# Optimization experiments

Measured on AMD Instinct MI355X. Metric: run time of the kernel, lower is better.

The kernel has to match this reference:

```python
import jax, jax.numpy as jnp
import numpy as np

N_NODES = 50000

def sage_conv(x, src, dst, W_l, b_l, W_r):
    # mean-aggregate neighbor features x[src] at dst, then lin_l(agg)+lin_r(x)
    msgs = x[src]                                       # [E, d]
    agg = jax.ops.segment_sum(msgs, dst, num_segments=N_NODES)
    cnt = jax.ops.segment_sum(jnp.ones((src.shape[0],), x.dtype), dst, num_segments=N_NODES)
    agg = agg / jnp.maximum(cnt, 1.0)[:, None]          # [N, d]
    return agg @ W_l.T + b_l + x @ W_r.T


def setup_inputs() -> dict:
    key = jax.random.key(0)
    ks = jax.random.split(key, 10)
    in_c, hid, out_c = 128, 128, 64
    x = jax.random.normal(ks[0], (N_NODES, in_c), dtype=jnp.float32)
    edge_index = jax.random.randint(ks[1], (2, 800000), 0, N_NODES, dtype=jnp.int64)
    s = 1.0 / np.sqrt(in_c)
    W1_l = jax.random.uniform(ks[2], (hid, in_c), minval=-s, maxval=s)
    b1 = jax.random.uniform(ks[3], (hid,), minval=-s, maxval=s)
    W1_r = jax.random.uniform(ks[4], (hid, in_c), minval=-s, maxval=s)
    s = 1.0 / np.sqrt(hid)
    W2_l = jax.random.uniform(ks[5], (hid, hid), minval=-s, maxval=s)
    b2 = jax.random.uniform(ks[6], (hid,), minval=-s, maxval=s)
    W2_r = jax.random.uniform(ks[7], (hid, hid), minval=-s, maxval=s)
    W3 = jax.random.uniform(ks[8], (out_c, hid), minval=-s, maxval=s)
    b3 = jax.random.uniform(ks[9], (out_c,), minval=-s, maxval=s)
    return {"x": x, "edge_index": edge_index, "W1_l": W1_l, "b1": b1, "W1_r": W1_r,
            "W2_l": W2_l, "b2": b2, "W2_r": W2_r, "W3": W3, "b3": b3}


def reference(x, edge_index, W1_l, b1, W1_r, W2_l, b2, W2_r, W3, b3):
    src, dst = edge_index[0], edge_index[1]
    h = jax.nn.relu(sage_conv(x, src, dst, W1_l, b1, W1_r))
    h = jax.nn.relu(sage_conv(h, src, dst, W2_l, b2, W2_r))
    return h @ W3.T + b3
```

## Files before the change

### kernel.cpp

```cpp
#include <hip/hip_runtime.h>

#define FDIM 128

typedef __attribute__((ext_vector_type(8))) short bf16x8;
typedef __attribute__((ext_vector_type(4))) float f32x4;

static __device__ __forceinline__ ushort f2bf(float f) {
    uint u = __float_as_uint(f);
    uint r = (u + 0x7FFF + ((u >> 16) & 1)) >> 16;
    return (ushort)r;
}
static __device__ __forceinline__ uint packbf(float lo, float hi) {
    return (uint)f2bf(lo) | ((uint)f2bf(hi) << 16);
}
static __device__ __forceinline__ float bflo(uint v) { return __uint_as_float(v << 16); }
static __device__ __forceinline__ float bfhi(uint v) { return __uint_as_float(v & 0xFFFF0000u); }

#define ACC8(A, V) do { \
    A[0] += bflo((V).x); A[1] += bfhi((V).x); \
    A[2] += bflo((V).y); A[3] += bfhi((V).y); \
    A[4] += bflo((V).z); A[5] += bfhi((V).z); \
    A[6] += bflo((V).w); A[7] += bfhi((V).w); } while (0)


__global__ void prep_kernel(const float* __restrict__ x, ushort* __restrict__ xb, int nx8,
                            const float* __restrict__ W1l, const float* __restrict__ W1r,
                            const float* __restrict__ W2l, const float* __restrict__ W2r,
                            const float* __restrict__ W3, ushort* __restrict__ wbuf,
                            const int* __restrict__ dst, int E, int* __restrict__ bcnt,
                            int* __restrict__ hdone, int* __restrict__ bbase,
                            int* __restrict__ bcur, int nb, int nconv, int nhist) {
    const int b = blockIdx.x;
    const int tid = threadIdx.x;
    if (b < nconv) {
        int i = b * 256 + tid;
        if (i < nx8) {
            const float* s = x + (size_t)i * 8;
            float4 a = *(const float4*)(s);
            float4 c = *(const float4*)(s + 4);
            uint4 o;
            o.x = packbf(a.x, a.y); o.y = packbf(a.z, a.w);
            o.z = packbf(c.x, c.y); o.w = packbf(c.z, c.w);
            *(uint4*)(xb + (size_t)i * 8) = o;
        }
    } else if (b < nconv + 36) {
        int c = (b - nconv) * 256 + tid;
        const float* s; ushort* d;
        if (c < 2048)      { s = W1l + (size_t)c * 8;          d = wbuf + (size_t)c * 8; }
        else if (c < 4096) { s = W1r + (size_t)(c - 2048) * 8; d = wbuf + 16384 + (size_t)(c - 2048) * 8; }
        else if (c < 6144) { s = W2l + (size_t)(c - 4096) * 8; d = wbuf + 32768 + (size_t)(c - 4096) * 8; }
        else if (c < 8192) { s = W2r + (size_t)(c - 6144) * 8; d = wbuf + 49152 + (size_t)(c - 6144) * 8; }
        else               { s = W3  + (size_t)(c - 8192) * 8; d = wbuf + 65536 + (size_t)(c - 8192) * 8; }
        float4 a = *(const float4*)(s);
        float4 cc = *(const float4*)(s + 4);
        uint4 o;
        o.x = packbf(a.x, a.y); o.y = packbf(a.z, a.w);
        o.z = packbf(cc.x, cc.y); o.w = packbf(cc.z, cc.w);
        *(uint4*)d = o;
    } else {
        __shared__ int lh[256];
        __shared__ int isLast;
        int hb = b - nconv - 36;
        lh[tid] = 0;
        __syncthreads();
        #pragma unroll
        for (int k = 0; k < 8; ++k) {
            int e = hb * 2048 + k * 256 + tid;
            if (e < E) atomicAdd(&lh[dst[e] >> 8], 1);
        }
        __syncthreads();
        if (lh[tid]) atomicAdd(&bcnt[tid], lh[tid]);
        __syncthreads();
        if (tid == 0) {
            __threadfence();
            isLast = (atomicAdd(hdone, 1) == nhist - 1);
        }
        __syncthreads();
        if (isLast && tid < 64) {
            __threadfence();
            volatile int* vb = bcnt;
            const int i0 = tid * 4;
            int v0 = (i0 + 0 < nb) ? vb[i0 + 0] : 0;
            int v1 = (i0 + 1 < nb) ? vb[i0 + 1] : 0;
            int v2 = (i0 + 2 < nb) ? vb[i0 + 2] : 0;
            int v3 = (i0 + 3 < nb) ? vb[i0 + 3] : 0;
            int s = v0 + v1 + v2 + v3;
            int incl = s;
            #pragma unroll
            for (int d = 1; d < 64; d <<= 1) {
                int t = __shfl_up(incl, d);
                if (tid >= d) incl += t;
            }
            int excl = incl - s;
            int e0 = excl, e1 = excl + v0, e2 = e1 + v1, e3 = e2 + v2;
            if (i0 + 0 < nb) { bbase[i0 + 0] = e0; bcur[i0 + 0] = e0; }
            if (i0 + 1 < nb) { bbase[i0 + 1] = e1; bcur[i0 + 1] = e1; }
            if (i0 + 2 < nb) { bbase[i0 + 2] = e2; bcur[i0 + 2] = e2; }
            if (i0 + 3 < nb) { bbase[i0 + 3] = e3; bcur[i0 + 3] = e3; }
            int total = __shfl(incl, 63);
            if (tid == 0) bbase[nb] = total;
        }
    }
}


__global__ void pair_scatter(const int* __restrict__ src, const int* __restrict__ dst,
                             int* __restrict__ bcur, uint* __restrict__ pairs, int E) {
    __shared__ int lh[256];
    __shared__ int gb[256];
    const int tid = threadIdx.x;
    lh[tid] = 0;
    __syncthreads();
    int ss[8], dd[8], sl[8];
    #pragma unroll
    for (int k = 0; k < 8; ++k) {
        int e = blockIdx.x * 2048 + k * 256 + tid;
        if (e < E) {
            ss[k] = src[e];
            dd[k] = dst[e];
            sl[k] = atomicAdd(&lh[dd[k] >> 8], 1);
        } else dd[k] = -1;
    }
    __syncthreads();
    if (lh[tid]) gb[tid] = atomicAdd(&bcur[tid], lh[tid]);
    __syncthreads();
    #pragma unroll
    for (int k = 0; k < 8; ++k) {
        if (dd[k] >= 0)
            pairs[gb[dd[k] >> 8] + sl[k]] = (uint)ss[k] | ((uint)(dd[k] & 255) << 24);
    }
}


__global__ void bucket_csr(const uint* __restrict__ pairs, const int* __restrict__ bbase,
                           int* __restrict__ off, int* __restrict__ csr, int N) {
    __shared__ int cnt[256];
    __shared__ int base[256];
    __shared__ int cur[256];
    const int b = blockIdx.x;
    const int tid = threadIdx.x;
    const int p0 = bbase[b], p1 = bbase[b + 1];
    cnt[tid] = 0;
    __syncthreads();
    for (int p = p0 + tid; p < p1; p += 256) atomicAdd(&cnt[pairs[p] >> 24], 1);
    __syncthreads();
    if (tid < 64) {
        int i0 = tid * 4;
        int v0 = cnt[i0], v1 = cnt[i0 + 1], v2 = cnt[i0 + 2], v3 = cnt[i0 + 3];
        int s = v0 + v1 + v2 + v3;
        int incl = s;
        #pragma unroll
        for (int d = 1; d < 64; d <<= 1) {
            int t = __shfl_up(incl, d);
            if (tid >= d) incl += t;
        }
        int excl = incl - s;
        base[i0] = excl; base[i0 + 1] = excl + v0;
        base[i0 + 2] = excl + v0 + v1; base[i0 + 3] = excl + v0 + v1 + v2;
        cur[i0] = base[i0]; cur[i0 + 1] = base[i0 + 1];
        cur[i0 + 2] = base[i0 + 2]; cur[i0 + 3] = base[i0 + 3];
    }
    __syncthreads();
    int node = (b << 8) + tid;
    if (node <= N) off[node] = p0 + base[tid];
    for (int p = p0 + tid; p < p1; p += 256) {
        uint e = pairs[p];
        int slot = atomicAdd(&cur[e >> 24], 1);
        csr[p0 + slot] = (int)(e & 0xFFFFFF);
    }
}


template<int HEAD>
__global__ void fused_sage(const ushort* __restrict__ feat, const int* __restrict__ off,
                           const int* __restrict__ csr,
                           const ushort* __restrict__ Wl, const ushort* __restrict__ Wr,
                           const float* __restrict__ bias,
                           const ushort* __restrict__ W3, const float* __restrict__ b3,
                           ushort* __restrict__ hout, float* __restrict__ fout, int n) {
    __shared__ __align__(16) ushort As[32 * FDIM];
    __shared__ __align__(16) ushort Xs[32 * FDIM];
    const int row0 = blockIdx.x * 32;
    const int lane = threadIdx.x & 63;
    const int wid  = threadIdx.x >> 6;

    const int offv = off[min(row0 + wid * 8 + min(lane, 8), n)];

    const float4 z4 = make_float4(0.f, 0.f, 0.f, 0.f);
    #pragma unroll
    for (int i = 0; i < 2; ++i) {
        int s = threadIdx.x + i * 256;
        int r = s >> 4, cch = s & 15;
        int row = row0 + r;
        float4 vx = (row < n) ? *(const float4*)(feat + (size_t)row * FDIM + cch * 8) : z4;
        *(float4*)(Xs + (r * 16 + (cch ^ (r & 7))) * 8) = vx;
    }

    const int g = lane >> 4;
    const int c = lane & 15;
    #define LDROW(s) (*(const uint4*)(feat + (size_t)(s) * FDIM + c * 8))

    #pragma unroll
    for (int i = 0; i < 4; ++i) {
        const int rA = wid * 8 + 2 * i;
        const int nodeA = row0 + rA, nodeB = nodeA + 1;
        const int j0A = __shfl(offv, 2 * i), j1A = __shfl(offv, 2 * i + 1);
        const int j1B = __shfl(offv, 2 * i + 2);
        float a[8] = {0.f, 0.f, 0.f, 0.f, 0.f, 0.f, 0.f, 0.f};
        float bacc[8] = {0.f, 0.f, 0.f, 0.f, 0.f, 0.f, 0.f, 0.f};
        int jA = j0A + g, jB = j1A + g;
        for (; jA + 12 < j1A && jB + 12 < j1B; jA += 16, jB += 16) {
            int sA0 = csr[jA], sA1 = csr[jA + 4], sA2 = csr[jA + 8], sA3 = csr[jA + 12];
            int sB0 = csr[jB], sB1 = csr[jB + 4], sB2 = csr[jB + 8], sB3 = csr[jB + 12];
            uint4 vA0 = LDROW(sA0), vA1 = LDROW(sA1), vA2 = LDROW(sA2), vA3 = LDROW(sA3);
            uint4 vB0 = LDROW(sB0), vB1 = LDROW(sB1), vB2 = LDROW(sB2), vB3 = LDROW(sB3);
            ACC8(a, vA0); ACC8(a, vA1); ACC8(a, vA2); ACC8(a, vA3);
            ACC8(bacc, vB0); ACC8(bacc, vB1); ACC8(bacc, vB2); ACC8(bacc, vB3);
        }
        for (; jA + 12 < j1A; jA += 16) {
            int s0 = csr[jA], s1 = csr[jA + 4], s2 = csr[jA + 8], s3 = csr[jA + 12];
            uint4 v0 = LDROW(s0), v1 = LDROW(s1), v2 = LDROW(s2), v3 = LDROW(s3);
            ACC8(a, v0); ACC8(a, v1); ACC8(a, v2); ACC8(a, v3);
        }
        for (; jA + 4 < j1A; jA += 8) {
            int s0 = csr[jA], s1 = csr[jA + 4];
            uint4 v0 = LDROW(s0), v1 = LDROW(s1);
            ACC8(a, v0); ACC8(a, v1);
        }
        for (; jA < j1A; jA += 4) {
            int s0 = csr[jA];
            uint4 v0 = LDROW(s0);
            ACC8(a, v0);
        }
        for (; jB + 12 < j1B; jB += 16) {
            int s0 = csr[jB], s1 = csr[jB + 4], s2 = csr[jB + 8], s3 = csr[jB + 12];
            uint4 v0 = LDROW(s0), v1 = LDROW(s1), v2 = LDROW(s2), v3 = LDROW(s3);
            ACC8(bacc, v0); ACC8(bacc, v1); ACC8(bacc, v2); ACC8(bacc, v3);
        }
        for (; jB + 4 < j1B; jB += 8) {
            int s0 = csr[jB], s1 = csr[jB + 4];
            uint4 v0 = LDROW(s0), v1 = LDROW(s1);
            ACC8(bacc, v0); ACC8(bacc, v1);
        }
        for (; jB < j1B; jB += 4) {
            int s0 = csr[jB];
            uint4 v0 = LDROW(s0);
            ACC8(bacc, v0);
        }
        #pragma unroll
        for (int k = 0; k < 8; ++k) {
            a[k] += __shfl_xor(a[k], 16);
            bacc[k] += __shfl_xor(bacc[k], 16);
            a[k] += __shfl_xor(a[k], 32);
            bacc[k] += __shfl_xor(bacc[k], 32);
        }
        if (g == 0) {
            float invA = (nodeA < n) ? 1.0f / fmaxf((float)(j1A - j0A), 1.0f) : 0.f;
            float invB = (nodeB < n) ? 1.0f / fmaxf((float)(j1B - j1A), 1.0f) : 0.f;
            uint4 oA, oB;
            oA.x = packbf(a[0] * invA, a[1] * invA);
            oA.y = packbf(a[2] * invA, a[3] * invA);
            oA.z = packbf(a[4] * invA, a[5] * invA);
            oA.w = packbf(a[6] * invA, a[7] * invA);
            oB.x = packbf(bacc[0] * invB, bacc[1] * invB);
            oB.y = packbf(bacc[2] * invB, bacc[3] * invB);
            oB.z = packbf(bacc[4] * invB, bacc[5] * invB);
            oB.w = packbf(bacc[6] * invB, bacc[7] * invB);
            *(uint4*)(As + (rA * 16 + (c ^ (rA & 7))) * 8) = oA;
            *(uint4*)(As + ((rA + 1) * 16 + (c ^ ((rA + 1) & 7))) * 8) = oB;
        }
    }
    #undef LDROW
    __syncthreads();

    const int wrow = wid & 1;
    const int wcol = wid >> 1;
    const int lr = lane & 15;
    const int lk = lane >> 4;

    f32x4 acc[4];
    #pragma unroll
    for (int t = 0; t < 4; ++t) acc[t] = (f32x4){0.f, 0.f, 0.f, 0.f};

    const int arow = wrow * 16 + lr;
    #pragma unroll
    for (int ks = 0; ks < 4; ++ks) {
        bf16x8 a = *(const bf16x8*)(As + (arow * 16 + ((ks * 4 + lk) ^ (arow & 7))) * 8);
        #pragma unroll
        for (int t = 0; t < 4; ++t) {
            int wr = wcol * 64 + t * 16 + lr;
            bf16x8 bb = *(const bf16x8*)(Wl + (size_t)wr * FDIM + ks * 32 + lk * 8);
            acc[t] = __builtin_amdgcn_mfma_f32_16x16x32_bf16(a, bb, acc[t], 0, 0, 0);
        }
    }
    #pragma unroll
    for (int ks = 0; ks < 4; ++ks) {
        bf16x8 a = *(const bf16x8*)(Xs + (arow * 16 + ((ks * 4 + lk) ^ (arow & 7))) * 8);
        #pragma unroll
        for (int t = 0; t < 4; ++t) {
            int wr = wcol * 64 + t * 16 + lr;
            bf16x8 bb = *(const bf16x8*)(Wr + (size_t)wr * FDIM + ks * 32 + lk * 8);
            acc[t] = __builtin_amdgcn_mfma_f32_16x16x32_bf16(a, bb, acc[t], 0, 0, 0);
        }
    }

    if (HEAD == 0) {
        #pragma unroll
        for (int t = 0; t < 4; ++t) {
            int col = wcol * 64 + t * 16 + lr;
            float bc = bias[col];
            #pragma unroll
            for (int j = 0; j < 4; ++j) {
                int row = row0 + wrow * 16 + lk * 4 + j;
                if (row < n) {
                    float v = fmaxf(acc[t][j] + bc, 0.f);
                    hout[(size_t)row * FDIM + col] = f2bf(v);
                }
            }
        }
    } else {
        __syncthreads();
        #pragma unroll
        for (int t = 0; t < 4; ++t) {
            int col = wcol * 64 + t * 16 + lr;
            float bc = bias[col];
            #pragma unroll
            for (int j = 0; j < 4; ++j) {
                int r = wrow * 16 + lk * 4 + j;
                float v = fmaxf(acc[t][j] + bc, 0.f);
                As[(r * 16 + ((col >> 3) ^ (r & 7))) * 8 + (col & 7)] = f2bf(v);
            }
        }
        __syncthreads();

        f32x4 acc2[2];
        #pragma unroll
        for (int t = 0; t < 2; ++t) acc2[t] = (f32x4){0.f, 0.f, 0.f, 0.f};

        #pragma unroll
        for (int ks = 0; ks < 4; ++ks) {
            bf16x8 a = *(const bf16x8*)(As + (arow * 16 + ((ks * 4 + lk) ^ (arow & 7))) * 8);
            #pragma unroll
            for (int t = 0; t < 2; ++t) {
                int wr = wcol * 32 + t * 16 + lr;
                bf16x8 bb = *(const bf16x8*)(W3 + (size_t)wr * FDIM + ks * 32 + lk * 8);
                acc2[t] = __builtin_amdgcn_mfma_f32_16x16x32_bf16(a, bb, acc2[t], 0, 0, 0);
            }
        }

        #pragma unroll
        for (int t = 0; t < 2; ++t) {
            int col = wcol * 32 + t * 16 + lr;
            float bc = b3[col];
            #pragma unroll
            for (int j = 0; j < 4; ++j) {
                int row = row0 + wrow * 16 + lk * 4 + j;
                if (row < n) fout[(size_t)row * 64 + col] = acc2[t][j] + bc;
            }
        }
    }
}


extern "C" void kernel_launch(void* const* d_in, const int* in_sizes, int n_in,
                              void* d_out, int out_size, void* d_ws, size_t ws_size,
                              hipStream_t stream) {
    const float* x   = (const float*)d_in[0];
    const int*   ei  = (const int*)d_in[1];
    const float* W1l = (const float*)d_in[2];
    const float* b1  = (const float*)d_in[3];
    const float* W1r = (const float*)d_in[4];
    const float* W2l = (const float*)d_in[5];
    const float* b2  = (const float*)d_in[6];
    const float* W2r = (const float*)d_in[7];
    const float* W3  = (const float*)d_in[8];
    const float* b3  = (const float*)d_in[9];
    float* out = (float*)d_out;

    const int N = in_sizes[0] / FDIM;
    const int E = in_sizes[1] / 2;
    const int* src = ei;
    const int* dst = ei + E;
    const int NBK = (N + 255) >> 8;

    char* ws = (char*)d_ws;
    size_t p = 0;
    auto alloc = [&](size_t bytes) {
        char* q = ws + p;
        p += (bytes + 255) & ~(size_t)255;
        return q;
    };
    int* ctrl    = (int*)alloc(272 * 4);
    int* bcnt    = ctrl;
    int* hdone   = ctrl + 256;
    int* bbase   = (int*)alloc(260 * 4);
    int* bcur    = (int*)alloc(256 * 4);
    uint* pairs  = (uint*)alloc((size_t)E * 4);
    int* csr     = (int*)alloc((size_t)E * 4);
    int* off     = (int*)alloc((size_t)(N + 1) * 4);
    ushort* xb   = (ushort*)alloc((size_t)N * FDIM * 2);
    ushort* h1b  = (ushort*)alloc((size_t)N * FDIM * 2);
    ushort* wbuf = (ushort*)alloc(73728 * 2);
    ushort* w1l = wbuf, *w1r = wbuf + 16384, *w2l = wbuf + 32768,
           *w2r = wbuf + 49152, *w3 = wbuf + 65536;

    hipMemsetAsync(ctrl, 0, 257 * 4, stream);

    const int nx8   = N * FDIM / 8;
    const int nconv = (nx8 + 255) / 256;
    const int nhist = (E + 2047) / 2048;
    prep_kernel<<<nconv + 36 + nhist, 256, 0, stream>>>(
        x, xb, nx8, W1l, W1r, W2l, W2r, W3, wbuf, dst, E, bcnt,
        hdone, bbase, bcur, NBK, nconv, nhist);
    pair_scatter<<<(E + 2047) / 2048, 256, 0, stream>>>(src, dst, bcur, pairs, E);
    bucket_csr<<<NBK, 256, 0, stream>>>(pairs, bbase, off, csr, N);

    const int lgrid = (N + 31) / 32;
    fused_sage<0><<<lgrid, 256, 0, stream>>>(xb, off, csr, w1l, w1r, b1,
                                             (const ushort*)nullptr, (const float*)nullptr,
                                             h1b, (float*)nullptr, N);
    fused_sage<1><<<lgrid, 256, 0, stream>>>(h1b, off, csr, w2l, w2r, b2,
                                             w3, b3, (ushort*)nullptr, out, N);
}
```

Before: 199.8 us.

## Halve rows per block in fused SAGE and split lin_l/lin_r across waves

Each block now handles 16 nodes instead of 32, so there are twice as many blocks, and each wave gathers one node at a time instead of two interleaved nodes. In the GEMM stage, half the waves compute agg@Wl and the other half x@Wr, and the partial sums are combined through a new float shared-memory buffer. Launch bounds request 8 blocks per CU. The aim is more occupancy and better load balance for the memory-latency-bound gather, at the cost of an extra shared buffer, an extra sync, and less memory-level parallelism per wave from dropping the dual-node interleave.

```diff
diff --git a/kernel.cpp b/kernel.cpp
--- a/kernel.cpp
+++ b/kernel.cpp
@@ -171,192 +171,142 @@
 }
 
 
+#define PS 132
+
 template<int HEAD>
-__global__ void fused_sage(const ushort* __restrict__ feat, const int* __restrict__ off,
-                           const int* __restrict__ csr,
-                           const ushort* __restrict__ Wl, const ushort* __restrict__ Wr,
-                           const float* __restrict__ bias,
-                           const ushort* __restrict__ W3, const float* __restrict__ b3,
-                           ushort* __restrict__ hout, float* __restrict__ fout, int n) {
-    __shared__ __align__(16) ushort As[32 * FDIM];
-    __shared__ __align__(16) ushort Xs[32 * FDIM];
-    const int row0 = blockIdx.x * 32;
+__global__ __launch_bounds__(256, 8)
+void fused_sage(const ushort* __restrict__ feat, const int* __restrict__ off,
+                const int* __restrict__ csr,
+                const ushort* __restrict__ Wl, const ushort* __restrict__ Wr,
+                const float* __restrict__ bias,
+                const ushort* __restrict__ W3, const float* __restrict__ b3,
+                ushort* __restrict__ hout, float* __restrict__ fout, int n) {
+    __shared__ __align__(16) ushort As[16 * FDIM];
+    __shared__ __align__(16) ushort Xs[16 * FDIM];
+    __shared__ __align__(16) float psum[16 * PS];
+    const int row0 = blockIdx.x * 16;
     const int lane = threadIdx.x & 63;
     const int wid  = threadIdx.x >> 6;
 
-    const int offv = off[min(row0 + wid * 8 + min(lane, 8), n)];
-
-    const float4 z4 = make_float4(0.f, 0.f, 0.f, 0.f);
-    #pragma unroll
-    for (int i = 0; i < 2; ++i) {
-        int s = threadIdx.x + i * 256;
-        int r = s >> 4, cch = s & 15;
+    {
+        int r = threadIdx.x >> 4, cch = threadIdx.x & 15;
         int row = row0 + r;
-        float4 vx = (row < n) ? *(const float4*)(feat + (size_t)row * FDIM + cch * 8) : z4;
+        float4 vx = make_float4(0.f, 0.f, 0.f, 0.f);
+        if (row < n) vx = *(const float4*)(feat + (size_t)row * FDIM + cch * 8);
         *(float4*)(Xs + (r * 16 + (cch ^ (r & 7))) * 8) = vx;
     }
 
     const int g = lane >> 4;
     const int c = lane & 15;
     #define LDROW(s) (*(const uint4*)(feat + (size_t)(s) * FDIM + c * 8))
-
-    #pragma unroll
     for (int i = 0; i < 4; ++i) {
-        const int rA = wid * 8 + 2 * i;
-        const int nodeA = row0 + rA, nodeB = nodeA + 1;
-        const int j0A = __shfl(offv, 2 * i), j1A = __shfl(offv, 2 * i + 1);
-        const int j1B = __shfl(offv, 2 * i + 2);
+        const int r = wid * 4 + i;
+        const int node = row0 + r;
         float a[8] = {0.f, 0.f, 0.f, 0.f, 0.f, 0.f, 0.f, 0.f};
-        float bacc[8] = {0.f, 0.f, 0.f, 0.f, 0.f, 0.f, 0.f, 0.f};
-        int jA = j0A + g, jB = j1A + g;
-        for (; jA + 12 < j1A && jB + 12 < j1B; jA += 16, jB += 16) {
-            int sA0 = csr[jA], sA1 = csr[jA + 4], sA2 = csr[jA + 8], sA3 = csr[jA + 12];
-            int sB0 = csr[jB], sB1 = csr[jB + 4], sB2 = csr[jB + 8], sB3 = csr[jB + 12];
-            uint4 vA0 = LDROW(sA0), vA1 = LDROW(sA1), vA2 = LDROW(sA2), vA3 = LDROW(sA3);
-            uint4 vB0 = LDROW(sB0), vB1 = LDROW(sB1), vB2 = LDROW(sB2), vB3 = LDROW(sB3);
-            ACC8(a, vA0); ACC8(a, vA1); ACC8(a, vA2); ACC8(a, vA3);
-            ACC8(bacc, vB0); ACC8(bacc, vB1); ACC8(bacc, vB2); ACC8(bacc, vB3);
-        }
-        for (; jA + 12 < j1A; jA += 16) {
-            int s0 = csr[jA], s1 = csr[jA + 4], s2 = csr[jA + 8], s3 = csr[jA + 12];
-            uint4 v0 = LDROW(s0), v1 = LDROW(s1), v2 = LDROW(s2), v3 = LDROW(s3);
-            ACC8(a, v0); ACC8(a, v1); ACC8(a, v2); ACC8(a, v3);
-        }
-        for (; jA + 4 < j1A; jA += 8) {
-            int s0 = csr[jA], s1 = csr[jA + 4];
-            uint4 v0 = LDROW(s0), v1 = LDROW(s1);
-            ACC8(a, v0); ACC8(a, v1);
-        }
-        for (; jA < j1A; jA += 4) {
-            int s0 = csr[jA];
-            uint4 v0 = LDROW(s0);
-            ACC8(a, v0);
-        }
-        for (; jB + 12 < j1B; jB += 16) {
-            int s0 = csr[jB], s1 = csr[jB + 4], s2 = csr[jB + 8], s3 = csr[jB + 12];
-            uint4 v0 = LDROW(s0), v1 = LDROW(s1), v2 = LDROW(s2), v3 = LDROW(s3);
-            ACC8(bacc, v0); ACC8(bacc, v1); ACC8(bacc, v2); ACC8(bacc, v3);
-        }
-        for (; jB + 4 < j1B; jB += 8) {
-            int s0 = csr[jB], s1 = csr[jB + 4];
-            uint4 v0 = LDROW(s0), v1 = LDROW(s1);
-            ACC8(bacc, v0); ACC8(bacc, v1);
-        }
-        for (; jB < j1B; jB += 4) {
-            int s0 = csr[jB];
-            uint4 v0 = LDROW(s0);
-            ACC8(bacc, v0);
+        float inv = 0.f;
+        if (node < n) {
+            const int j0 = off[node], j1 = off[node + 1];
+            int j = j0 + g;
+            for (; j + 12 < j1; j += 16) {
+                int s0 = csr[j], s1 = csr[j + 4], s2 = csr[j + 8], s3 = csr[j + 12];
+                uint4 v0 = LDROW(s0), v1 = LDROW(s1), v2 = LDROW(s2), v3 = LDROW(s3);
+                ACC8(a, v0); ACC8(a, v1); ACC8(a, v2); ACC8(a, v3);
+            }
+            for (; j + 4 < j1; j += 8) {
+                int s0 = csr[j], s1 = csr[j + 4];
+                uint4 v0 = LDROW(s0), v1 = LDROW(s1);
+                ACC8(a, v0); ACC8(a, v1);
+            }
+            for (; j < j1; j += 4) {
+                uint4 v0 = LDROW(csr[j]);
+                ACC8(a, v0);
+            }
+            inv = 1.0f / fmaxf((float)(j1 - j0), 1.0f);
         }
         #pragma unroll
         for (int k = 0; k < 8; ++k) {
             a[k] += __shfl_xor(a[k], 16);
-            bacc[k] += __shfl_xor(bacc[k], 16);
             a[k] += __shfl_xor(a[k], 32);
-            bacc[k] += __shfl_xor(bacc[k], 32);
         }
         if (g == 0) {
-            float invA = (nodeA < n) ? 1.0f / fmaxf((float)(j1A - j0A), 1.0f) : 0.f;
-            float invB = (nodeB < n) ? 1.0f / fmaxf((float)(j1B - j1A), 1.0f) : 0.f;
-            uint4 oA, oB;
-            oA.x = packbf(a[0] * invA, a[1] * invA);
-            oA.y = packbf(a[2] * invA, a[3] * invA);
-            oA.z = packbf(a[4] * invA, a[5] * invA);
-            oA.w = packbf(a[6] * invA, a[7] * invA);
-            oB.x = packbf(bacc[0] * invB, bacc[1] * invB);
-            oB.y = packbf(bacc[2] * invB, bacc[3] * invB);
-            oB.z = packbf(bacc[4] * invB, bacc[5] * invB);
-            oB.w = packbf(bacc[6] * invB, bacc[7] * invB);
-            *(uint4*)(As + (rA * 16 + (c ^ (rA & 7))) * 8) = oA;
-            *(uint4*)(As + ((rA + 1) * 16 + (c ^ ((rA + 1) & 7))) * 8) = oB;
+            uint4 o;
+            o.x = packbf(a[0] * inv, a[1] * inv);
+            o.y = packbf(a[2] * inv, a[3] * inv);
+            o.z = packbf(a[4] * inv, a[5] * inv);
+            o.w = packbf(a[6] * inv, a[7] * inv);
+            *(uint4*)(As + (r * 16 + (c ^ (r & 7))) * 8) = o;
         }
     }
     #undef LDROW
     __syncthreads();
 
-    const int wrow = wid & 1;
-    const int wcol = wid >> 1;
+    const int op   = wid >> 1;
+    const int half = wid & 1;
     const int lr = lane & 15;
     const int lk = lane >> 4;
+    const ushort* Atile = op ? Xs : As;
+    const ushort* W     = op ? Wr : Wl;
 
     f32x4 acc[4];
     #pragma unroll
     for (int t = 0; t < 4; ++t) acc[t] = (f32x4){0.f, 0.f, 0.f, 0.f};
 
-    const int arow = wrow * 16 + lr;
     #pragma unroll
     for (int ks = 0; ks < 4; ++ks) {
-        bf16x8 a = *(const bf16x8*)(As + (arow * 16 + ((ks * 4 + lk) ^ (arow & 7))) * 8);
+        bf16x8 a = *(const bf16x8*)(Atile + (lr * 16 + ((ks * 4 + lk) ^ (lr & 7))) * 8);
         #pragma unroll
         for (int t = 0; t < 4; ++t) {
-            int wr = wcol * 64 + t * 16 + lr;
-            bf16x8 bb = *(const bf16x8*)(Wl + (size_t)wr * FDIM + ks * 32 + lk * 8);
+            int wr = half * 64 + t * 16 + lr;
+            bf16x8 bb = *(const bf16x8*)(W + (size_t)wr * FDIM + ks * 32 + lk * 8);
             acc[t] = __builtin_amdgcn_mfma_f32_16x16x32_bf16(a, bb, acc[t], 0, 0, 0);
         }
     }
-    #pragma unroll
-    for (int ks = 0; ks < 4; ++ks) {
-        bf16x8 a = *(const bf16x8*)(Xs + (arow * 16 + ((ks * 4 + lk) ^ (arow & 7))) * 8);
+
+    if (op == 1) {
         #pragma unroll
         for (int t = 0; t < 4; ++t) {
-            int wr = wcol * 64 + t * 16 + lr;
-            bf16x8 bb = *(const bf16x8*)(Wr + (size_t)wr * FDIM + ks * 32 + lk * 8);
-            acc[t] = __builtin_amdgcn_mfma_f32_16x16x32_bf16(a, bb, acc[t], 0, 0, 0);
-        }
-    }
-
-    if (HEAD == 0) {
+            #pragma unroll
+            for (int j = 0; j < 4; ++j)
+                psum[(lk * 4 + j) * PS + half * 64 + t * 16 + lr] = acc[t][j];
+        }
+    }
+    __syncthreads();
+
+    if (op == 0) {
         #pragma unroll
         for (int t = 0; t < 4; ++t) {
-            int col = wcol * 64 + t * 16 + lr;
+            int col = half * 64 + t * 16 + lr;
             float bc = bias[col];
             #pragma unroll
             for (int j = 0; j < 4; ++j) {
-                int row = row0 + wrow * 16 + lk * 4 + j;
-                if (row < n) {
-                    float v = fmaxf(acc[t][j] + bc, 0.f);
-                    hout[(size_t)row * FDIM + col] = f2bf(v);
+                int r = lk * 4 + j;
+                float v = fmaxf(acc[t][j] + psum[r * PS + col] + bc, 0.f);
+                if (HEAD == 0) {
+                    int row = row0 + r;
+                    if (row < n) hout[(size_t)row * FDIM + col] = f2bf(v);
+                } else {
+                    As[(r * 16 + ((col >> 3) ^ (r & 7))) * 8 + (col & 7)] = f2bf(v);
                 }
             }
         }
-    } else {
-        __syncthreads();
-        #pragma unroll
-        for (int t = 0; t < 4; ++t) {
-            int col = wcol * 64 + t * 16 + lr;
-            float bc = bias[col];
-            #pragma unroll
-            for (int j = 0; j < 4; ++j) {
-                int r = wrow * 16 + lk * 4 + j;
-                float v = fmaxf(acc[t][j] + bc, 0.f);
-                As[(r * 16 + ((col >> 3) ^ (r & 7))) * 8 + (col & 7)] = f2bf(v);
-            }
-        }
-        __syncthreads();
-
-        f32x4 acc2[2];
-        #pragma unroll
-        for (int t = 0; t < 2; ++t) acc2[t] = (f32x4){0.f, 0.f, 0.f, 0.f};
-
+    }
+
+    if (HEAD == 1) {
+        __syncthreads();
+        f32x4 acc2 = (f32x4){0.f, 0.f, 0.f, 0.f};
         #pragma unroll
         for (int ks = 0; ks < 4; ++ks) {
-            bf16x8 a = *(const bf16x8*)(As + (arow * 16 + ((ks * 4 + lk) ^ (arow & 7))) * 8);
-            #pragma unroll
-            for (int t = 0; t < 2; ++t) {
-                int wr = wcol * 32 + t * 16 + lr;
-                bf16x8 bb = *(const bf16x8*)(W3 + (size_t)wr * FDIM + ks * 32 + lk * 8);
-                acc2[t] = __builtin_amdgcn_mfma_f32_16x16x32_bf16(a, bb, acc2[t], 0, 0, 0);
-            }
-        }
-
-        #pragma unroll
-        for (int t = 0; t < 2; ++t) {
-            int col = wcol * 32 + t * 16 + lr;
-            float bc = b3[col];
-            #pragma unroll
-            for (int j = 0; j < 4; ++j) {
-                int row = row0 + wrow * 16 + lk * 4 + j;
-                if (row < n) fout[(size_t)row * 64 + col] = acc2[t][j] + bc;
-            }
+            bf16x8 a = *(const bf16x8*)(As + (lr * 16 + ((ks * 4 + lk) ^ (lr & 7))) * 8);
+            int wr = wid * 16 + lr;
+            bf16x8 bb = *(const bf16x8*)(W3 + (size_t)wr * FDIM + ks * 32 + lk * 8);
+            acc2 = __builtin_amdgcn_mfma_f32_16x16x32_bf16(a, bb, acc2, 0, 0, 0);
+        }
+        int col = wid * 16 + lr;
+        float bc = b3[col];
+        #pragma unroll
+        for (int j = 0; j < 4; ++j) {
+            int row = row0 + lk * 4 + j;
+            if (row < n) fout[(size_t)row * 64 + col] = acc2[j] + bc;
         }
     }
 }
@@ -415,7 +365,7 @@
     pair_scatter<<<(E + 2047) / 2048, 256, 0, stream>>>(src, dst, bcur, pairs, E);
     bucket_csr<<<NBK, 256, 0, stream>>>(pairs, bbase, off, csr, N);
 
-    const int lgrid = (N + 31) / 32;
+    const int lgrid = (N + 15) / 16;
     fused_sage<0><<<lgrid, 256, 0, stream>>>(xb, off, csr, w1l, w1r, b1,
                                              (const ushort*)nullptr, (const float*)nullptr,
                                              h1b, (float*)nullptr, N);
```

New measurement: 171.8 us. 1.16x faster.
